# Kernel tuning notes

Hardware: AMD Instinct MI355X
Metric: run time of the kernel (lower is better)

## Reference

```python
import jax, jax.numpy as jnp
import numpy as np

N, E, B = 30000, 100000, 1024
FXD, FXT, D, H, NOUT = 78, 954, 128, 10, 2


def setup_inputs() -> dict:
    key = jax.random.key(0)
    ks = jax.random.split(key, 24)
    rn = lambda i, shape, s=0.05: jax.random.normal(ks[i], shape, dtype=jnp.float32) * s
    z = lambda shape: jnp.zeros(shape, dtype=jnp.float32)
    batch = ((jnp.arange(N) * B) // N).astype(jnp.int32)  # sorted, every graph id present
    return {
        "x1": rn(0, (N, FXD), 1.0),
        "edge_index1": jax.random.randint(ks[1], (2, E), 0, N, dtype=jnp.int32),
        "batch1": batch,
        "x2": rn(2, (N, FXD), 1.0),
        "edge_index2": jax.random.randint(ks[3], (2, E), 0, N, dtype=jnp.int32),
        "batch2": batch,
        "cell": jax.random.uniform(ks[4], (B, FXT), dtype=jnp.float32),
        "W1": rn(5, (FXD, H * D)), "a_src1": rn(6, (1, H, D)), "a_dst1": rn(7, (1, H, D)), "b1": z((H * D,)),
        # GATConv2: 1280 -> 128, 1 head
        "W2": rn(8, (H * D, D)), "a_src2": rn(9, (1, 1, D)), "a_dst2": rn(10, (1, 1, D)), "b2": z((D,)),
        "Wg": rn(11, (D, D)), "bg": z((D,)),
        "Wr1": rn(12, (FXT, 2048)), "br1": z((2048,)),
        "Wr2": rn(13, (2048, 512)), "br2": z((512,)),
        "Wr3": rn(14, (512, 2 * D)), "br3": z((2 * D,)),
        "Wf1": rn(15, (4 * D, 1024)), "bf1": z((1024,)),
        "Wf2": rn(16, (1024, 512)), "bf2": z((512,)),
        "Wf3": rn(17, (512, 128)), "bf3": z((128,)),
        "Wo": rn(18, (128, NOUT)), "bo": z((NOUT,)),
    }


def gat_conv(x, src, dst, W, a_src, a_dst, bias, heads, ch):
    """PyG GATConv (v1), self-loops already included in src/dst. Concat heads."""
    n = x.shape[0]
    h = (x @ W).reshape(n, heads, ch)                      # [N,H,C]
    alpha_s = jnp.sum(h * a_src, axis=-1)                  # [N,H]
    alpha_d = jnp.sum(h * a_dst, axis=-1)                  # [N,H]
    e = jax.nn.leaky_relu(alpha_s[src] + alpha_d[dst], 0.2)  # [E',H]
    emax = jax.ops.segment_max(e, dst, num_segments=n)     # segment softmax over dst
    ex = jnp.exp(e - emax[dst])
    denom = jax.ops.segment_sum(ex, dst, num_segments=n)
    alpha = ex / (denom[dst] + 1e-16)                      # [E',H]
    msg = h[src] * alpha[:, :, None]                       # [E',H,C]
    out = jax.ops.segment_sum(msg, dst, num_segments=n)    # [N,H,C]
    return out.reshape(n, heads * ch) + bias


def _l2norm(x):
    return x / jnp.maximum(jnp.linalg.norm(x, axis=1, keepdims=True), 1e-12)


def reference(x1, edge_index1, batch1, x2, edge_index2, batch2, cell,
              W1, a_src1, a_dst1, b1, W2, a_src2, a_dst2, b2, Wg, bg,
              Wr1, br1, Wr2, br2, Wr3, br3, Wf1, bf1, Wf2, bf2, Wf3, bf3, Wo, bo):
    def branch(x, ei, batch):
        n = x.shape[0]
        loops = jnp.arange(n, dtype=ei.dtype)              # add_self_loops=True
        src = jnp.concatenate([ei[0], loops])
        dst = jnp.concatenate([ei[1], loops])
        h = jax.nn.elu(gat_conv(x, src, dst, W1, a_src1, a_dst1, b1, H, D))
        h = jax.nn.elu(gat_conv(h, src, dst, W2, a_src2, a_dst2, b2, 1, D))
        g = jax.ops.segment_max(h, batch, num_segments=B)  # global_max_pool
        return jax.nn.relu(g @ Wg + bg)

    v1 = branch(x1, edge_index1, batch1)
    v2 = branch(x2, edge_index2, batch2)
    c = _l2norm(cell)
    c = jax.nn.relu(c @ Wr1 + br1)
    c = jax.nn.relu(c @ Wr2 + br2)
    c = jax.nn.relu(c @ Wr3 + br3)
    xc = _l2norm(jnp.concatenate([v1, v2, c], axis=1))
    xc = jax.nn.relu(xc @ Wf1 + bf1)
    xc = jax.nn.relu(xc @ Wf2 + bf2)
    xc = jax.nn.relu(xc @ Wf3 + bf3)
    return xc @ Wo + bo
```

## Files before the change

kernel.cpp:

```cpp
#include <hip/hip_runtime.h>
#include <math.h>

typedef unsigned short ushort_t;
typedef __attribute__((ext_vector_type(8))) short short8;
typedef __attribute__((ext_vector_type(8))) unsigned short ushort8v;
typedef __attribute__((ext_vector_type(4))) float float4v;
typedef __attribute__((ext_vector_type(4))) unsigned short ushort4v;

#define MPAD 30016
#define H1STR 136

__device__ __forceinline__ float lrelu02(float v){ return v > 0.f ? v : 0.2f*v; }
__device__ __forceinline__ float elu_fast(float v){ return v > 0.f ? v : (__expf(v) - 1.f); }

__device__ __forceinline__ ushort_t f2bf(float x){
  unsigned u = __float_as_uint(x);
  return (ushort_t)((u + 0x7fffu + ((u >> 16) & 1u)) >> 16);
}
__device__ __forceinline__ float bf2f(ushort_t h){ return __uint_as_float(((unsigned)h) << 16); }

__device__ __forceinline__ unsigned encf(float f){
  unsigned u = __float_as_uint(f);
  return (u & 0x80000000u) ? ~u : (u | 0x80000000u);
}
__device__ __forceinline__ float decf(unsigned u){
  return __uint_as_float((u >> 31) ? (u & 0x7FFFFFFFu) : ~u);
}

__device__ __forceinline__ void gll16(const void* g, void* l){
  __builtin_amdgcn_global_load_lds((const __attribute__((address_space(1))) void*)g,
                                   (__attribute__((address_space(3))) void*)l, 16, 0, 0);
}

__global__ void fill_int_k(int* p, int v, int n){
  int i = blockIdx.x*blockDim.x + threadIdx.x;
  if (i < n) p[i] = v;
}

__global__ void hist2_k(const int* __restrict__ ei1, const int* __restrict__ ei2,
                        int E, int N, int* deg){
  int idx = blockIdx.x*blockDim.x + threadIdx.x;
  if (idx < 2*E){
    int br = idx / E, e = idx - br*E;
    const int* ei = br ? ei2 : ei1;
    atomicAdd(&deg[br*N + ei[E + e]], 1);
  }
}

__global__ __launch_bounds__(1024)
void scanA_k(const int* __restrict__ deg, int* __restrict__ rowptr, int* __restrict__ bsum, int n){
  int br = blockIdx.y;
  int t = threadIdx.x;
  int i = blockIdx.x*1024 + t;
  __shared__ int s[1024];
  int v = (i < n) ? deg[br*n + i] : 0;
  s[t] = v; __syncthreads();
  for (int off = 1; off < 1024; off <<= 1){
    int x = (t >= off) ? s[t - off] : 0;
    __syncthreads();
    s[t] += x;
    __syncthreads();
  }
  if (i < n) rowptr[br*(n+1) + i] = s[t] - v;
  if (t == 1023) bsum[br*gridDim.x + blockIdx.x] = s[1023];
}

__global__ void scanB_k(int* bsum, int nb){
  int br = threadIdx.x;
  if (br < 2){
    int run = 0;
    for (int i = 0; i < nb; ++i){ int v = bsum[br*nb + i]; bsum[br*nb + i] = run; run += v; }
  }
}

__global__ __launch_bounds__(1024)
void scanC_k(const int* __restrict__ bsum, int* __restrict__ rowptr, int* __restrict__ cursor,
             int n, int nb, int total){
  int br = blockIdx.y;
  int i = blockIdx.x*1024 + threadIdx.x;
  int add = bsum[br*nb + blockIdx.x];
  if (i < n){
    int nv = rowptr[br*(n+1) + i] + add;
    rowptr[br*(n+1) + i] = nv;
    cursor[br*n + i] = nv;
  }
  if (i == 0) rowptr[br*(n+1) + n] = total;
}

__global__ void fill_csr2_k(const int* __restrict__ ei1, const int* __restrict__ ei2,
                            int E, int N, int* cursor, int* csr){
  int idx = blockIdx.x*blockDim.x + threadIdx.x;
  if (idx < 2*E){
    int br = idx / E, e = idx - br*E;
    const int* ei = br ? ei2 : ei1;
    int dst = ei[E + e];
    int pos = atomicAdd(&cursor[br*N + dst], 1);
    csr[br*(E+N) + pos] = ei[e];
  }
}

__global__ void self_loop2_k(int* cursor, int* csr, int E, int N){
  int idx = blockIdx.x*blockDim.x + threadIdx.x;
  if (idx < 2*N){
    int br = idx / N, i = idx - br*N;
    int pos = atomicAdd(&cursor[br*N + i], 1);
    csr[br*(E+N) + pos] = i;
  }
}

__global__ void mkattn_k(const float* __restrict__ W1, const float* __restrict__ a_src1,
                         const float* __restrict__ a_dst1,
                         const float* __restrict__ W2, const float* __restrict__ a_src2,
                         const float* __restrict__ a_dst2,
                         float* As, float* Ad, float* vs, float* vd){
  int idx = blockIdx.x*blockDim.x + threadIdx.x;
  if (idx < 780){
    int f = idx / 10, h = idx % 10;
    float ss = 0.f, sd = 0.f;
    for (int c = 0; c < 128; ++c){
      float w = W1[f*1280 + h*128 + c];
      ss += w * a_src1[h*128 + c];
      sd += w * a_dst1[h*128 + c];
    }
    As[idx] = ss; Ad[idx] = sd;
  } else if (idx < 2060){
    int k = idx - 780;
    float ss = 0.f, sd = 0.f;
    for (int c = 0; c < 128; ++c){
      float w = W2[k*128 + c];
      ss += w * a_src2[c]; sd += w * a_dst2[c];
    }
    vs[k] = ss; vd[k] = sd;
  }
}

__global__ __launch_bounds__(256)
void alpha1b_k(const float* __restrict__ x1, const float* __restrict__ x2,
               const float* __restrict__ As, const float* __restrict__ Ad,
               float* as1, float* ad1, int n){
  __shared__ float sAs[780], sAd[780];
  int t = threadIdx.x;
  for (int k = t; k < 780; k += 256){ sAs[k] = As[k]; sAd[k] = Ad[k]; }
  __syncthreads();
  int idx = blockIdx.x*256 + t;
  if (idx >= 2*n) return;
  int br = idx / n, i = idx - br*n;
  const float* xr = (br ? x2 : x1) + (size_t)i*78;
  float ss[10], sd[10];
  #pragma unroll
  for (int h = 0; h < 10; ++h){ ss[h] = 0.f; sd[h] = 0.f; }
  for (int f = 0; f < 78; ++f){
    float xv = xr[f];
    #pragma unroll
    for (int h = 0; h < 10; ++h){
      ss[h] += xv * sAs[f*10 + h];
      sd[h] += xv * sAd[f*10 + h];
    }
  }
  #pragma unroll
  for (int h = 0; h < 10; ++h){
    as1[(size_t)idx*10 + h] = ss[h];
    ad1[(size_t)idx*10 + h] = sd[h];
  }
}

__global__ __launch_bounds__(64)
void gat1_agg_k(const int* __restrict__ rowptr2, const int* __restrict__ csr2,
                const float* __restrict__ x1, const float* __restrict__ x2,
                const float* __restrict__ as1b, const float* __restrict__ ad1b,
                ushort_t* __restrict__ yh, int n, int E){
  int gi = blockIdx.x;
  int br = (gi >= n) ? 1 : 0;
  int i = gi - br*n;
  int t = threadIdx.x;
  const int* rowptr = rowptr2 + (size_t)br*(n+1);
  const int* csr    = csr2 + (size_t)br*(E+n);
  const float* x    = br ? x2 : x1;
  const float* as1  = as1b + (size_t)br*n*10;
  ushort_t* yb      = yh + (size_t)br*10*MPAD*96;

  __shared__ float adi[10], rden[10], wE[10], xs[78];
  int beg = rowptr[i], end = rowptr[i+1];
  if (t < 10) adi[t] = ad1b[(size_t)gi*10 + t];
  __syncthreads();
  float den = 0.f;
  float acc[13];
  int hh[13], cc[13];
  #pragma unroll
  for (int k = 0; k < 13; ++k){
    acc[k] = 0.f;
    int j = t + 64*k;
    hh[k] = (j < 780) ? (j/78) : 0;
    cc[k] = (j < 780) ? (j%78) : 0;
  }
  for (int e = beg; e < end; ++e){
    int s = csr[e];
    if (t < 10){
      float w = __expf(lrelu02(as1[(size_t)s*10 + t] + adi[t]));
      wE[t] = w; den += w;
    }
    for (int c = t; c < 78; c += 64) xs[c] = x[(size_t)s*78 + c];
    __syncthreads();
    #pragma unroll
    for (int k = 0; k < 13; ++k){
      int j = t + 64*k;
      if (j < 780) acc[k] += wE[hh[k]] * xs[cc[k]];
    }
    __syncthreads();
  }
  if (t < 10) rden[t] = 1.f/(den + 1e-16f);
  __syncthreads();
  #pragma unroll
  for (int k = 0; k < 13; ++k){
    int j = t + 64*k;
    if (j < 780) yb[((size_t)hh[k]*MPAD + i)*96 + cc[k]] = f2bf(acc[k]*rden[hh[k]]);
  }
  for (int p = t; p < 180; p += 64){
    int h = p/18, c = 78 + p%18;
    yb[((size_t)h*MPAD + i)*96 + c] = 0;
  }
}

__global__ __launch_bounds__(256)
void branch_conv_k(const ushort_t* __restrict__ yall,
                   const ushort_t* __restrict__ W1h, const ushort_t* __restrict__ W1l,
                   const ushort_t* __restrict__ W2h, const ushort_t* __restrict__ W2l,
                   const float* __restrict__ b1, const float* __restrict__ vs,
                   const float* __restrict__ vd,
                   float* __restrict__ h2all, float* __restrict__ as2all,
                   float* __restrict__ ad2all, int M){
  const int NBLK = MPAD/64;
  int br = blockIdx.x / NBLK;
  int bi = blockIdx.x - br*NBLK;
  const ushort_t* y = yall + (size_t)br*10*MPAD*96;
  float* h2  = h2all + (size_t)br*MPAD*128;
  float* as2 = as2all + (size_t)br*MPAD;
  float* ad2 = ad2all + (size_t)br*MPAD;

  __shared__ ushort_t stage[2][10240];
  __shared__ ushort_t h1t[64*H1STR];
  __shared__ float red[256];

  int tid = threadIdx.x, lane = tid & 63, wave = tid >> 6;
  int row0 = bi*64;
  int wm = (wave & 1)*32, wn = (wave >> 1)*64;
  int lr = lane & 15, quad = lane >> 4;
  int sr = lane >> 2;
  int skc = (((lane & 3) ^ ((lane >> 3) & 3)) * 8);
  int qs  = (quad ^ ((lr >> 1) & 3)) * 8;

  float4v acc2[2][4];
  #pragma unroll
  for (int i = 0; i < 2; ++i)
    #pragma unroll
    for (int j = 0; j < 4; ++j)
      acc2[i][j] = (float4v){0.f, 0.f, 0.f, 0.f};
  float rps[8], rpd[8];
  #pragma unroll
  for (int z = 0; z < 8; ++z){ rps[z] = 0.f; rpd[z] = 0.f; }

  for (int h = 0; h < 10; ++h){
    const ushort_t* gA   = y   + ((size_t)h*MPAD + row0 + wave*16 + sr)*96 + skc;
    const ushort_t* gB0h = W1h + ((size_t)(h*128 + wave*32      + sr))*96 + skc;
    const ushort_t* gB1h = W1h + ((size_t)(h*128 + wave*32 + 16 + sr))*96 + skc;
    const ushort_t* gB0l = W1l + ((size_t)(h*128 + wave*32      + sr))*96 + skc;
    const ushort_t* gB1l = W1l + ((size_t)(h*128 + wave*32 + 16 + sr))*96 + skc;
    const ushort_t* gC0h = W2h + ((size_t)(wave*32      + sr))*1280 + h*128 + skc;
    const ushort_t* gC1h = W2h + ((size_t)(wave*32 + 16 + sr))*1280 + h*128 + skc;
    const ushort_t* gC0l = W2l + ((size_t)(wave*32      + sr))*1280 + h*128 + skc;
    const ushort_t* gC1l = W2l + ((size_t)(wave*32 + 16 + sr))*1280 + h*128 + skc;

    auto issue1 = [&](int p, int kt){
      ushort_t* st = &stage[p][0];
      gll16(gA   + kt, st + wave*512);
      gll16(gB0h + kt, st + 2048 + wave*1024);
      gll16(gB1h + kt, st + 2048 + wave*1024 + 512);
      gll16(gB0l + kt, st + 6144 + wave*1024);
      gll16(gB1l + kt, st + 6144 + wave*1024 + 512);
    };
    auto issue2 = [&](int p, int kt){
      ushort_t* st = &stage[p][0];
      gll16(gC0h + kt, st + 2048 + wave*1024);
      gll16(gC1h + kt, st + 2048 + wave*1024 + 512);
      gll16(gC0l + kt, st + 6144 + wave*1024);
      gll16(gC1l + kt, st + 6144 + wave*1024 + 512);
    };

    __syncthreads();
    issue1(0, 0);
    float4v acc1[2][4];
    #pragma unroll
    for (int i = 0; i < 2; ++i)
      #pragma unroll
      for (int j = 0; j < 4; ++j)
        acc1[i][j] = (float4v){0.f, 0.f, 0.f, 0.f};
    int p = 0;
    #pragma unroll
    for (int it = 0; it < 3; ++it){
      __syncthreads();
      if (it < 2) issue1(p ^ 1, (it + 1)*32);
      const ushort_t* sm = &stage[p][0];
      short8 af[2], bhf[4], blf[4];
      #pragma unroll
      for (int t2 = 0; t2 < 2; ++t2)
        af[t2] = *(const short8*)&sm[(wm + t2*16 + lr)*32 + qs];
      #pragma unroll
      for (int j = 0; j < 4; ++j){
        int nb = (wn + j*16 + lr)*32 + qs;
        bhf[j] = *(const short8*)&sm[2048 + nb];
        blf[j] = *(const short8*)&sm[6144 + nb];
      }
      #pragma unroll
      for (int i = 0; i < 2; ++i)
        #pragma unroll
        for (int j = 0; j < 4; ++j){
          acc1[i][j] = __builtin_amdgcn_mfma_f32_16x16x32_bf16(af[i], blf[j], acc1[i][j], 0, 0, 0);
          acc1[i][j] = __builtin_amdgcn_mfma_f32_16x16x32_bf16(af[i], bhf[j], acc1[i][j], 0, 0, 0);
        }
      p ^= 1;
    }

    #pragma unroll
    for (int j = 0; j < 4; ++j){
      int col = wn + j*16 + lr;
      float bv  = b1[h*128 + col];
      float vsv = vs[h*128 + col];
      float vdv = vd[h*128 + col];
      #pragma unroll
      for (int i = 0; i < 2; ++i){
        #pragma unroll
        for (int r = 0; r < 4; ++r){
          float v = elu_fast(acc1[i][j][r] + bv);
          h1t[(wm + i*16 + quad*4 + r)*H1STR + col] = f2bf(v);
          rps[i*4 + r] += v * vsv;
          rpd[i*4 + r] += v * vdv;
        }
      }
    }
    __syncthreads();

    issue2(0, 0);
    p = 0;
    #pragma unroll
    for (int it = 0; it < 4; ++it){
      __syncthreads();
      if (it < 3) issue2(p ^ 1, (it + 1)*32);
      const ushort_t* sm = &stage[p][0];
      int kt = it*32;
      short8 af[2], bhf[4], blf[4];
      #pragma unroll
      for (int t2 = 0; t2 < 2; ++t2)
        af[t2] = *(const short8*)&h1t[(wm + t2*16 + lr)*H1STR + kt + quad*8];
      #pragma unroll
      for (int j = 0; j < 4; ++j){
        int nb = (wn + j*16 + lr)*32 + qs;
        bhf[j] = *(const short8*)&sm[2048 + nb];
        blf[j] = *(const short8*)&sm[6144 + nb];
      }
      #pragma unroll
      for (int i = 0; i < 2; ++i)
        #pragma unroll
        for (int j = 0; j < 4; ++j){
          acc2[i][j] = __builtin_amdgcn_mfma_f32_16x16x32_bf16(af[i], blf[j], acc2[i][j], 0, 0, 0);
          acc2[i][j] = __builtin_amdgcn_mfma_f32_16x16x32_bf16(af[i], bhf[j], acc2[i][j], 0, 0, 0);
        }
      p ^= 1;
    }
  }

  #pragma unroll
  for (int j = 0; j < 4; ++j){
    int col = wn + j*16 + lr;
    #pragma unroll
    for (int i = 0; i < 2; ++i){
      #pragma unroll
      for (int r = 0; r < 4; ++r){
        int row = row0 + wm + i*16 + quad*4 + r;
        if (row < M) h2[(size_t)row*128 + col] = acc2[i][j][r];
      }
    }
  }
  __syncthreads();
  #pragma unroll
  for (int z = 0; z < 8; ++z){
    float a = rps[z], d = rpd[z];
    #pragma unroll
    for (int mk = 1; mk <= 8; mk <<= 1){
      a += __shfl_xor(a, mk);
      d += __shfl_xor(d, mk);
    }
    if (lr == 0){
      int i = z >> 2, r = z & 3;
      int row = wm + i*16 + quad*4 + r;
      red[row*2 + (wave >> 1)] = a;
      red[128 + row*2 + (wave >> 1)] = d;
    }
  }
  __syncthreads();
  if (tid < 64){
    int grow = row0 + tid;
    if (grow < M){
      as2[grow] = red[tid*2] + red[tid*2 + 1];
      ad2[grow] = red[128 + tid*2] + red[128 + tid*2 + 1];
    }
  }
}

__global__ __launch_bounds__(64)
void gat2_agg_k(const int* __restrict__ rowptr2, const int* __restrict__ csr2,
                const float* __restrict__ h2all, const float* __restrict__ as2all,
                const float* __restrict__ ad2all, const float* __restrict__ b2,
                const int* __restrict__ batch1, const int* __restrict__ batch2,
                unsigned* __restrict__ poolKey, int n, int E, int Bg){
  int gi = blockIdx.x;
  int br = (gi >= n) ? 1 : 0;
  int i = gi - br*n;
  int t = threadIdx.x;
  const int* rowptr = rowptr2 + (size_t)br*(n+1);
  const int* csr    = csr2 + (size_t)br*(E+n);
  const float* h2   = h2all + (size_t)br*MPAD*128;
  const float* as2  = as2all + (size_t)br*MPAD;
  float adi = ad2all[(size_t)br*MPAD + i];
  int beg = rowptr[i], end = rowptr[i+1];
  float den = 0.f, a0 = 0.f, a1 = 0.f;
  for (int e = beg; e < end; ++e){
    int s = csr[e];
    float w = __expf(lrelu02(as2[s] + adi));
    den += w;
    a0 += w * h2[(size_t)s*128 + t];
    a1 += w * h2[(size_t)s*128 + 64 + t];
  }
  float r = 1.f/(den + 1e-16f);
  float o0 = elu_fast(a0*r + b2[t]);
  float o1 = elu_fast(a1*r + b2[64 + t]);
  int g = (br ? batch2 : batch1)[i];
  unsigned* pk = poolKey + ((size_t)br*Bg + g)*128;
  atomicMax(&pk[t], encf(o0));
  atomicMax(&pk[64 + t], encf(o1));
}

__global__ void pool_decode_k(const unsigned* __restrict__ key,
                              ushort_t* __restrict__ ph, ushort_t* __restrict__ pl, int n){
  int i = blockIdx.x*blockDim.x + threadIdx.x;
  if (i < n){
    float v = decf(key[i]);
    ushort_t h = f2bf(v);
    ph[i] = h; pl[i] = f2bf(v - bf2f(h));
  }
}

__global__ __launch_bounds__(256)
void l2norm_split_k(const float* __restrict__ in, int cols, int Kp,
                    ushort_t* __restrict__ oh, ushort_t* __restrict__ ol){
  int r = blockIdx.x, t = threadIdx.x;
  __shared__ float s[256];
  __shared__ float scaleS;
  const float* rp = in + (size_t)r*cols;
  float p = 0.f;
  for (int k = t; k < cols; k += 256){ float v = rp[k]; p += v*v; }
  s[t] = p; __syncthreads();
  for (int o = 128; o > 0; o >>= 1){
    if (t < o) s[t] += s[t+o];
    __syncthreads();
  }
  if (t == 0) scaleS = 1.f / fmaxf(sqrtf(s[0]), 1e-12f);
  __syncthreads();
  float sc = scaleS;
  for (int k = t; k < Kp; k += 256){
    float v = (k < cols) ? rp[k]*sc : 0.f;
    ushort_t h = f2bf(v);
    size_t o2 = (size_t)r*Kp + k;
    oh[o2] = h; ol[o2] = f2bf(v - bf2f(h));
  }
}

__global__ __launch_bounds__(256)
void catnorm_k(const float* __restrict__ vall, const float* __restrict__ c3,
               ushort_t* __restrict__ oh, ushort_t* __restrict__ ol, int Bg){
  int r = blockIdx.x, t = threadIdx.x;
  __shared__ float s[256];
  __shared__ float scaleS;
  auto val = [&](int c)->float{
    if (c < 128) return vall[(size_t)r*128 + c];
    if (c < 256) return vall[((size_t)Bg + r)*128 + (c - 128)];
    return c3[(size_t)r*256 + (c - 256)];
  };
  float v0 = val(t), v1 = val(t + 256);
  s[t] = v0*v0 + v1*v1; __syncthreads();
  for (int o = 128; o > 0; o >>= 1){
    if (t < o) s[t] += s[t+o];
    __syncthreads();
  }
  if (t == 0) scaleS = 1.f / fmaxf(sqrtf(s[0]), 1e-12f);
  __syncthreads();
  float sc = scaleS;
  float a = v0*sc, b = v1*sc;
  ushort_t ha = f2bf(a), hb = f2bf(b);
  size_t o2 = (size_t)r*512;
  oh[o2 + t] = ha;       ol[o2 + t] = f2bf(a - bf2f(ha));
  oh[o2 + 256 + t] = hb; ol[o2 + 256 + t] = f2bf(b - bf2f(hb));
}

__global__ void act_split_k(const float* __restrict__ in, ushort_t* __restrict__ oh,
                            ushort_t* __restrict__ ol, int n){
  int i = blockIdx.x*blockDim.x + threadIdx.x;
  if (i < n){
    float v = fmaxf(in[i], 0.f);
    ushort_t h = f2bf(v);
    oh[i] = h; ol[i] = f2bf(v - bf2f(h));
  }
}

__device__ __forceinline__ void split_one(const float* __restrict__ W, int ldw, int colStride,
                                          int N, int K, int Np, int Kp,
                                          ushort_t* __restrict__ dh, ushort_t* __restrict__ dl,
                                          int idx){
  int n  = idx % Np;
  int r  = idx / Np;
  int k4 = r % (Kp >> 2);
  int b  = r / (Kp >> 2);
  size_t o = ((size_t)b*Np + n)*Kp + (size_t)k4*4;
  ushort4v hv, lv;
  #pragma unroll
  for (int kk = 0; kk < 4; ++kk){
    int k = k4*4 + kk;
    float v = (n < N && k < K) ? W[(size_t)k*ldw + (size_t)b*colStride + n] : 0.f;
    ushort_t h = f2bf(v);
    hv[kk] = h; lv[kk] = f2bf(v - bf2f(h));
  }
  *(ushort4v*)&dh[o] = hv;
  *(ushort4v*)&dl[o] = lv;
}

struct SplitTable {
  const float *W1, *W2, *Wg, *Wr1, *Wr2, *Wr3, *Wf1, *Wf2, *Wf3, *Wo;
  ushort_t *W1h,*W1l,*W2h,*W2l,*Wgh,*Wgl,*Wr1h,*Wr1l,*Wr2h,*Wr2l;
  ushort_t *Wr3h,*Wr3l,*Wf1h,*Wf1l,*Wf2h,*Wf2l,*Wf3h,*Wf3l,*Woh,*Wol;
};

__global__ void split_all_k(SplitTable T){
  int idx = blockIdx.x*blockDim.x + threadIdx.x;
  if      (idx <   30720) split_one(T.W1, 1280, 128, 128,   78,  128,   96, T.W1h, T.W1l, idx);
  else if (idx <   71680) split_one(T.W2,  128,   0, 128, 1280,  128, 1280, T.W2h, T.W2l, idx -   30720);
  else if (idx <   75776) split_one(T.Wg,  128,   0, 128,  128,  128,  128, T.Wgh, T.Wgl, idx -   71680);
  else if (idx <  567296) split_one(T.Wr1,2048,   0,2048,  954, 2048,  960, T.Wr1h,T.Wr1l,idx -   75776);
  else if (idx <  829440) split_one(T.Wr2, 512,   0, 512, 2048,  512, 2048, T.Wr2h,T.Wr2l,idx -  567296);
  else if (idx <  862208) split_one(T.Wr3, 256,   0, 256,  512,  256,  512, T.Wr3h,T.Wr3l,idx -  829440);
  else if (idx <  993280) split_one(T.Wf1,1024,   0,1024,  512, 1024,  512, T.Wf1h,T.Wf1l,idx -  862208);
  else if (idx < 1124352) split_one(T.Wf2, 512,   0, 512, 1024,  512, 1024, T.Wf2h,T.Wf2l,idx -  993280);
  else if (idx < 1140736) split_one(T.Wf3, 128,   0, 128,  512,  128,  512, T.Wf3h,T.Wf3l,idx - 1124352);
  else if (idx < 1142784) split_one(T.Wo,    2,   0,   2,  128,   64,  128, T.Woh, T.Wol, idx - 1140736);
}

__global__ __launch_bounds__(256)
void gemm_split(const ushort_t* __restrict__ Ahp, const ushort_t* __restrict__ Alp, int lda, long long sA,
                const ushort_t* __restrict__ Bhp, const ushort_t* __restrict__ Blp, int ldb, long long sB,
                float* __restrict__ C, ushort_t* __restrict__ Ch, ushort_t* __restrict__ Cl,
                int ldc, long long sC,
                const float* __restrict__ bias, int sBias,
                int M, int Nc, int K, int act, int outMode, int kSplit, int aSplit){
  int zb = blockIdx.z;
  int b = zb / kSplit, kc = zb - b*kSplit;
  Ahp += (long long)b*sA;
  Bhp += (long long)b*sB; Blp += (long long)b*sB;
  long long cOff = (long long)b*sC;
  int Kc = K / kSplit;
  int kb = kc*Kc;
  int nIter = Kc / 32;

  __shared__ ushort_t smem[18048];

  int tid = threadIdx.x, lane = tid & 63, wave = tid >> 6;
  int row0 = blockIdx.y*64, col0 = blockIdx.x*64;
  int wm = (wave & 1)*32, wn = (wave >> 1)*32;
  int lr = lane & 15, quad = lane >> 4;
  int qs = (quad ^ ((lr >> 1) & 3)) * 8;

  int srow = wave*16 + (lane >> 2);
  int skc  = (((lane & 3) ^ ((lane >> 3) & 3)) * 8);
  const ushort_t* gAh = Ahp + (long long)(row0 + srow)*lda + skc + kb;
  const ushort_t* gAl = aSplit ? (Alp + (long long)b*sA + (long long)(row0 + srow)*lda + skc + kb) : gAh;
  const ushort_t* gBh = Bhp + (long long)(col0 + srow)*ldb + skc + kb;
  const ushort_t* gBl = Blp + (long long)(col0 + srow)*ldb + skc + kb;

  float4v acc[2][2];
  #pragma unroll
  for (int i = 0; i < 2; ++i)
    #pragma unroll
    for (int j = 0; j < 2; ++j)
      acc[i][j] = (float4v){0.f, 0.f, 0.f, 0.f};

  auto issue = [&](int p, int kt){
    ushort_t* base = &smem[p*8192 + wave*512];
    gll16(gAh + kt, base);
    if (aSplit) gll16(gAl + kt, base + 2048);
    gll16(gBh + kt, base + 4096);
    gll16(gBl + kt, base + 6144);
  };

  issue(0, 0);
  int p = 0;
  for (int it = 0; it < nIter; ++it){
    __syncthreads();
    if (it + 1 < nIter) issue(p ^ 1, (it + 1)*32);
    const ushort_t* sm = &smem[p*8192];
    short8 ah[2], al[2], bh[2], bl[2];
    #pragma unroll
    for (int t2 = 0; t2 < 2; ++t2){
      int ao = (wm + t2*16 + lr)*32 + qs;
      int bo = (wn + t2*16 + lr)*32 + qs;
      ah[t2] = *(const short8*)&sm[ao];
      if (aSplit) al[t2] = *(const short8*)&sm[2048 + ao];
      bh[t2] = *(const short8*)&sm[4096 + bo];
      bl[t2] = *(const short8*)&sm[6144 + bo];
    }
    #pragma unroll
    for (int i = 0; i < 2; ++i)
      #pragma unroll
      for (int j = 0; j < 2; ++j){
        if (aSplit)
          acc[i][j] = __builtin_amdgcn_mfma_f32_16x16x32_bf16(al[i], bh[j], acc[i][j], 0, 0, 0);
        acc[i][j] = __builtin_amdgcn_mfma_f32_16x16x32_bf16(ah[i], bl[j], acc[i][j], 0, 0, 0);
        acc[i][j] = __builtin_amdgcn_mfma_f32_16x16x32_bf16(ah[i], bh[j], acc[i][j], 0, 0, 0);
      }
    p ^= 1;
  }
  __syncthreads();

  if (outMode == 0 || outMode == 2){
    #pragma unroll
    for (int j = 0; j < 2; ++j){
      int col = col0 + wn + j*16 + lr;
      if (col >= Nc) continue;
      float bv = (bias && kc == 0) ? bias[(long long)b*sBias + col] : 0.f;
      #pragma unroll
      for (int i = 0; i < 2; ++i){
        #pragma unroll
        for (int r = 0; r < 4; ++r){
          int row = row0 + wm + i*16 + quad*4 + r;
          if (row >= M) continue;
          float v = acc[i][j][r] + bv;
          if (act == 1) v = fmaxf(v, 0.f);
          else if (act == 2) v = elu_fast(v);
          long long o = cOff + (long long)row*ldc + col;
          if (outMode == 0) C[o] = v;
          else atomicAdd(&C[o], v);
        }
      }
    }
  } else {
    float* ftile = (float*)smem;
    #pragma unroll
    for (int i = 0; i < 2; ++i)
      #pragma unroll
      for (int j = 0; j < 2; ++j)
        #pragma unroll
        for (int r = 0; r < 4; ++r)
          ftile[(wm + i*16 + quad*4 + r)*68 + wn + j*16 + lr] = acc[i][j][r];
    __syncthreads();
    int row = tid >> 2, ch = (tid & 3)*16;
    int grow = row0 + row;
    if (grow < M){
      if (col0 + 64 <= Nc){
        long long o = cOff + (long long)grow*ldc + col0 + ch;
        #pragma unroll
        for (int g = 0; g < 2; ++g){
          ushort8v hv, lv;
          #pragma unroll
          for (int c = 0; c < 8; ++c){
            int cc2 = ch + g*8 + c;
            float v = ftile[row*68 + cc2];
            if (bias) v += bias[(long long)b*sBias + col0 + cc2];
            if (act == 1) v = fmaxf(v, 0.f);
            else if (act == 2) v = elu_fast(v);
            hv[c] = f2bf(v);
            lv[c] = f2bf(v - bf2f(hv[c]));
          }
          *(ushort8v*)&Ch[o + g*8] = hv;
          *(ushort8v*)&Cl[o + g*8] = lv;
        }
      } else {
        for (int c = 0; c < 16; ++c){
          int col = col0 + ch + c;
          if (col >= Nc) break;
          float v = ftile[row*68 + ch + c];
          if (bias) v += bias[(long long)b*sBias + col];
          if (act == 1) v = fmaxf(v, 0.f);
          else if (act == 2) v = elu_fast(v);
          long long o = cOff + (long long)grow*ldc + col;
          ushort_t h = f2bf(v);
          Ch[o] = h;
          Cl[o] = f2bf(v - bf2f(h));
        }
      }
    }
  }
}

extern "C" void kernel_launch(void* const* d_in, const int* in_sizes, int n_in,
                              void* d_out, int out_size, void* d_ws, size_t ws_size,
                              hipStream_t stream){
  const float* x1     = (const float*)d_in[0];
  const int*   ei1    = (const int*)  d_in[1];
  const int*   batch1 = (const int*)  d_in[2];
  const float* x2     = (const float*)d_in[3];
  const int*   ei2    = (const int*)  d_in[4];
  const int*   batch2 = (const int*)  d_in[5];
  const float* cell   = (const float*)d_in[6];
  const float* W1     = (const float*)d_in[7];
  const float* a_src1 = (const float*)d_in[8];
  const float* a_dst1 = (const float*)d_in[9];
  const float* b1     = (const float*)d_in[10];
  const float* W2     = (const float*)d_in[11];
  const float* a_src2 = (const float*)d_in[12];
  const float* a_dst2 = (const float*)d_in[13];
  const float* b2     = (const float*)d_in[14];
  const float* Wg     = (const float*)d_in[15];
  const float* bg     = (const float*)d_in[16];
  const float* Wr1    = (const float*)d_in[17];
  const float* br1    = (const float*)d_in[18];
  const float* Wr2    = (const float*)d_in[19];
  const float* br2    = (const float*)d_in[20];
  const float* Wr3    = (const float*)d_in[21];
  const float* br3    = (const float*)d_in[22];
  const float* Wf1    = (const float*)d_in[23];
  const float* bf1    = (const float*)d_in[24];
  const float* Wf2    = (const float*)d_in[25];
  const float* bf2    = (const float*)d_in[26];
  const float* Wf3    = (const float*)d_in[27];
  const float* bf3    = (const float*)d_in[28];
  const float* Wo     = (const float*)d_in[29];
  const float* bo     = (const float*)d_in[30];
  float* out = (float*)d_out;
  (void)n_in; (void)out_size; (void)ws_size;

  const int N  = in_sizes[0] / 78;
  const int E  = in_sizes[1] / 2;
  const int Bg = in_sizes[6] / 954;

  char* wsb = (char*)d_ws;
  size_t off = 0;
  auto alloc = [&](size_t bytes)->char*{
    char* p = wsb + off; off += ((bytes + 255)/256)*256; return p;
  };

  char* Yb = alloc((size_t)2*10*MPAD*96*2);
  ushort_t* yh = (ushort_t*)Yb;
  size_t yoff = 0;
  auto yalloc = [&](size_t bytes)->char*{
    char* p = Yb + yoff; yoff += ((bytes + 255)/256)*256; return p;
  };
  ushort_t* cnh  = (ushort_t*)yalloc((size_t)Bg*960*2);
  ushort_t* cnl  = (ushort_t*)yalloc((size_t)Bg*960*2);
  ushort_t* c1h  = (ushort_t*)yalloc((size_t)Bg*2048*2);
  ushort_t* c1l  = (ushort_t*)yalloc((size_t)Bg*2048*2);
  ushort_t* c2h  = (ushort_t*)yalloc((size_t)Bg*512*2);
  ushort_t* c2l  = (ushort_t*)yalloc((size_t)Bg*512*2);
  float*    c3   = (float*)   yalloc((size_t)Bg*256*4);
  ushort_t* xcnh = (ushort_t*)yalloc((size_t)Bg*512*2);
  ushort_t* xcnl = (ushort_t*)yalloc((size_t)Bg*512*2);
  ushort_t* t1h  = (ushort_t*)yalloc((size_t)Bg*1024*2);
  ushort_t* t1l  = (ushort_t*)yalloc((size_t)Bg*1024*2);
  ushort_t* t2h  = (ushort_t*)yalloc((size_t)Bg*512*2);
  ushort_t* t2l  = (ushort_t*)yalloc((size_t)Bg*512*2);
  ushort_t* t3h  = (ushort_t*)yalloc((size_t)Bg*128*2);
  ushort_t* t3l  = (ushort_t*)yalloc((size_t)Bg*128*2);
  ushort_t* pooledh = (ushort_t*)yalloc((size_t)2*Bg*128*2);
  ushort_t* pooledl = (ushort_t*)yalloc((size_t)2*Bg*128*2);
  float*    vall    = (float*)   yalloc((size_t)2*Bg*128*4);

  size_t zElems = (size_t)Bg*512 + (size_t)Bg*512 + (size_t)Bg*128 + (size_t)2*Bg*128;
  float* zbase = (float*)alloc(zElems*4);
  float* c2f = zbase;
  float* t2f = c2f + (size_t)Bg*512;
  float* t3f = t2f + (size_t)Bg*512;
  unsigned* poolKey = (unsigned*)(t3f + (size_t)Bg*128);

  float* h2  = (float*)alloc((size_t)2*MPAD*128*4);
  float* as2 = (float*)alloc((size_t)2*MPAD*4);
  float* ad2 = (float*)alloc((size_t)2*MPAD*4);

  ushort_t* W1th = (ushort_t*)alloc((size_t)10*128*96*2);
  ushort_t* W1tl = (ushort_t*)alloc((size_t)10*128*96*2);
  ushort_t* W2th = (ushort_t*)alloc((size_t)128*1280*2);
  ushort_t* W2tl = (ushort_t*)alloc((size_t)128*1280*2);
  ushort_t* Wgth = (ushort_t*)alloc((size_t)128*128*2);
  ushort_t* Wgtl = (ushort_t*)alloc((size_t)128*128*2);
  ushort_t* Wr1th= (ushort_t*)alloc((size_t)2048*960*2);
  ushort_t* Wr1tl= (ushort_t*)alloc((size_t)2048*960*2);
  ushort_t* Wr2th= (ushort_t*)alloc((size_t)512*2048*2);
  ushort_t* Wr2tl= (ushort_t*)alloc((size_t)512*2048*2);
  ushort_t* Wr3th= (ushort_t*)alloc((size_t)256*512*2);
  ushort_t* Wr3tl= (ushort_t*)alloc((size_t)256*512*2);
  ushort_t* Wf1th= (ushort_t*)alloc((size_t)1024*512*2);
  ushort_t* Wf1tl= (ushort_t*)alloc((size_t)1024*512*2);
  ushort_t* Wf2th= (ushort_t*)alloc((size_t)512*1024*2);
  ushort_t* Wf2tl= (ushort_t*)alloc((size_t)512*1024*2);
  ushort_t* Wf3th= (ushort_t*)alloc((size_t)128*512*2);
  ushort_t* Wf3tl= (ushort_t*)alloc((size_t)128*512*2);
  ushort_t* Woth = (ushort_t*)alloc((size_t)64*128*2);
  ushort_t* Wotl = (ushort_t*)alloc((size_t)64*128*2);

  float* as1b = (float*)alloc((size_t)2*N*10*4);
  float* ad1b = (float*)alloc((size_t)2*N*10*4);
  float* AsB  = (float*)alloc(780*4);
  float* AdB  = (float*)alloc(780*4);
  float* vs   = (float*)alloc(1280*4);
  float* vd   = (float*)alloc(1280*4);
  int* deg2    = (int*)alloc((size_t)2*N*4);
  int* rowptr2 = (int*)alloc((size_t)2*(N+1)*4);
  int* cursor2 = (int*)alloc((size_t)2*N*4);
  int* csr2    = (int*)alloc((size_t)2*(E+N)*4);
  int* bsum    = (int*)alloc((size_t)2*64*4);

  auto gemm = [&](const ushort_t* Ah_, const ushort_t* Al_, int lda, long long sA_,
                  const ushort_t* Bh_, const ushort_t* Bl_, int ldb, long long sB_,
                  float* C_, ushort_t* Ch_, ushort_t* Cl_, int ldc, long long sC_,
                  const float* bias_, int sBias_, int M_, int N_, int K_, int batch_,
                  int act_, int mode_, int kSplit_, int aSplit_){
    dim3 grid((N_ + 63)/64, (M_ + 63)/64, batch_*kSplit_);
    gemm_split<<<grid, 256, 0, stream>>>(Ah_, Al_, lda, sA_, Bh_, Bl_, ldb, sB_,
                                         C_, Ch_, Cl_, ldc, sC_, bias_, sBias_,
                                         M_, N_, K_, act_, mode_, kSplit_, aSplit_);
  };

  hipMemsetAsync(zbase, 0, zElems*4, stream);
  SplitTable T;
  T.W1 = W1; T.W2 = W2; T.Wg = Wg; T.Wr1 = Wr1; T.Wr2 = Wr2; T.Wr3 = Wr3;
  T.Wf1 = Wf1; T.Wf2 = Wf2; T.Wf3 = Wf3; T.Wo = Wo;
  T.W1h = W1th; T.W1l = W1tl; T.W2h = W2th; T.W2l = W2tl; T.Wgh = Wgth; T.Wgl = Wgtl;
  T.Wr1h = Wr1th; T.Wr1l = Wr1tl; T.Wr2h = Wr2th; T.Wr2l = Wr2tl;
  T.Wr3h = Wr3th; T.Wr3l = Wr3tl; T.Wf1h = Wf1th; T.Wf1l = Wf1tl;
  T.Wf2h = Wf2th; T.Wf2l = Wf2tl; T.Wf3h = Wf3th; T.Wf3l = Wf3tl;
  T.Woh = Woth; T.Wol = Wotl;
  split_all_k<<<(1142784 + 255)/256, 256, 0, stream>>>(T);
  mkattn_k<<<(2060 + 255)/256, 256, 0, stream>>>(W1, a_src1, a_dst1, W2, a_src2, a_dst2,
                                                 AsB, AdB, vs, vd);
  alpha1b_k<<<((2*N) + 255)/256, 256, 0, stream>>>(x1, x2, AsB, AdB, as1b, ad1b, N);

  const int NB = (N + 1023)/1024;
  fill_int_k<<<((2*N) + 255)/256, 256, 0, stream>>>(deg2, 1, 2*N);
  hist2_k<<<((2*E) + 255)/256, 256, 0, stream>>>(ei1, ei2, E, N, deg2);
  scanA_k<<<dim3(NB, 2), 1024, 0, stream>>>(deg2, rowptr2, bsum, N);
  scanB_k<<<1, 64, 0, stream>>>(bsum, NB);
  scanC_k<<<dim3(NB, 2), 1024, 0, stream>>>(bsum, rowptr2, cursor2, N, NB, E + N);
  fill_csr2_k<<<((2*E) + 255)/256, 256, 0, stream>>>(ei1, ei2, E, N, cursor2, csr2);
  self_loop2_k<<<((2*N) + 255)/256, 256, 0, stream>>>(cursor2, csr2, E, N);

  gat1_agg_k<<<2*N, 64, 0, stream>>>(rowptr2, csr2, x1, x2, as1b, ad1b, yh, N, E);
  branch_conv_k<<<2*(MPAD/64), 256, 0, stream>>>(yh, W1th, W1tl, W2th, W2tl,
                                                 b1, vs, vd, h2, as2, ad2, N);
  gat2_agg_k<<<2*N, 64, 0, stream>>>(rowptr2, csr2, h2, as2, ad2, b2,
                                     batch1, batch2, poolKey, N, E, Bg);
  pool_decode_k<<<((2*Bg*128) + 255)/256, 256, 0, stream>>>(poolKey, pooledh, pooledl, 2*Bg*128);
  gemm(pooledh, pooledl, 128, 0, Wgth, Wgtl, 128, 0,
       vall, nullptr, nullptr, 128, 0, bg, 0, 2*Bg, 128, 128, 1, 1, 0, 1, 1);

  l2norm_split_k<<<Bg, 256, 0, stream>>>(cell, 954, 960, cnh, cnl);
  gemm(cnh, cnl, 960, 0, Wr1th, Wr1tl, 960, 0, nullptr, c1h, c1l, 2048, 0,
       br1, 0, Bg, 2048, 960, 1, 1, 1, 1, 1);
  gemm(c1h, c1l, 2048, 0, Wr2th, Wr2tl, 2048, 0, c2f, nullptr, nullptr, 512, 0,
       br2, 0, Bg, 512, 2048, 1, 0, 2, 4, 1);
  act_split_k<<<((Bg*512) + 255)/256, 256, 0, stream>>>(c2f, c2h, c2l, Bg*512);
  gemm(c2h, c2l, 512, 0, Wr3th, Wr3tl, 512, 0, c3, nullptr, nullptr, 256, 0,
       br3, 0, Bg, 256, 512, 1, 1, 0, 1, 1);

  catnorm_k<<<Bg, 256, 0, stream>>>(vall, c3, xcnh, xcnl, Bg);
  gemm(xcnh, xcnl, 512, 0, Wf1th, Wf1tl, 512, 0, nullptr, t1h, t1l, 1024, 0,
       bf1, 0, Bg, 1024, 512, 1, 1, 1, 1, 1);
  gemm(t1h, t1l, 1024, 0, Wf2th, Wf2tl, 1024, 0, t2f, nullptr, nullptr, 512, 0,
       bf2, 0, Bg, 512, 1024, 1, 0, 2, 4, 1);
  act_split_k<<<((Bg*512) + 255)/256, 256, 0, stream>>>(t2f, t2h, t2l, Bg*512);
  gemm(t2h, t2l, 512, 0, Wf3th, Wf3tl, 512, 0, t3f, nullptr, nullptr, 128, 0,
       bf3, 0, Bg, 128, 512, 1, 0, 2, 4, 1);
  act_split_k<<<((Bg*128) + 255)/256, 256, 0, stream>>>(t3f, t3h, t3l, Bg*128);
  gemm(t3h, t3l, 128, 0, Woth, Wotl, 128, 0, out, nullptr, nullptr, 2, 0,
       bo, 0, Bg, 2, 128, 1, 0, 0, 1, 1);
}
```

Baseline: 601.0 us.

## Drop low-part bf16 split for GAT weights, store h2 as bf16, fuse CSR kernels

Removes the hi/lo bf16 split compensation for W1 and W2 in the fused branch convolution, which halves the MFMA count and the weight staging traffic there. The h2 intermediate is now stored as bf16 instead of fp32, cutting write and gather bandwidth in the second GAT aggregation. The degree fill kernel is folded into the memset plus a +1 in the scan, and the self-loop insertion is merged into the CSR fill kernel, saving launches. The cost is reduced precision in the GAT layers, which risks exceeding the accuracy tolerance.

```diff
diff --git a/kernel.cpp b/kernel.cpp
--- a/kernel.cpp
+++ b/kernel.cpp
@@ -30,11 +30,6 @@
 __device__ __forceinline__ void gll16(const void* g, void* l){
   __builtin_amdgcn_global_load_lds((const __attribute__((address_space(1))) void*)g,
                                    (__attribute__((address_space(3))) void*)l, 16, 0, 0);
-}
-
-__global__ void fill_int_k(int* p, int v, int n){
-  int i = blockIdx.x*blockDim.x + threadIdx.x;
-  if (i < n) p[i] = v;
 }
 
 __global__ void hist2_k(const int* __restrict__ ei1, const int* __restrict__ ei2,
@@ -53,7 +48,7 @@
   int t = threadIdx.x;
   int i = blockIdx.x*1024 + t;
   __shared__ int s[1024];
-  int v = (i < n) ? deg[br*n + i] : 0;
+  int v = (i < n) ? (deg[br*n + i] + 1) : 0;
   s[t] = v; __syncthreads();
   for (int off = 1; off < 1024; off <<= 1){
     int x = (t >= off) ? s[t - off] : 0;
@@ -96,13 +91,9 @@
     int dst = ei[E + e];
     int pos = atomicAdd(&cursor[br*N + dst], 1);
     csr[br*(E+N) + pos] = ei[e];
-  }
-}
-
-__global__ void self_loop2_k(int* cursor, int* csr, int E, int N){
-  int idx = blockIdx.x*blockDim.x + threadIdx.x;
-  if (idx < 2*N){
-    int br = idx / N, i = idx - br*N;
+  } else if (idx < 2*E + 2*N){
+    int r = idx - 2*E;
+    int br = r / N, i = r - br*N;
     int pos = atomicAdd(&cursor[br*N + i], 1);
     csr[br*(E+N) + pos] = i;
   }
@@ -223,21 +214,20 @@
 
 __global__ __launch_bounds__(256)
 void branch_conv_k(const ushort_t* __restrict__ yall,
-                   const ushort_t* __restrict__ W1h, const ushort_t* __restrict__ W1l,
-                   const ushort_t* __restrict__ W2h, const ushort_t* __restrict__ W2l,
+                   const ushort_t* __restrict__ W1h, const ushort_t* __restrict__ W2h,
                    const float* __restrict__ b1, const float* __restrict__ vs,
                    const float* __restrict__ vd,
-                   float* __restrict__ h2all, float* __restrict__ as2all,
+                   ushort_t* __restrict__ h2all, float* __restrict__ as2all,
                    float* __restrict__ ad2all, int M){
   const int NBLK = MPAD/64;
   int br = blockIdx.x / NBLK;
   int bi = blockIdx.x - br*NBLK;
   const ushort_t* y = yall + (size_t)br*10*MPAD*96;
-  float* h2  = h2all + (size_t)br*MPAD*128;
+  ushort_t* h2 = h2all + (size_t)br*MPAD*128;
   float* as2 = as2all + (size_t)br*MPAD;
   float* ad2 = ad2all + (size_t)br*MPAD;
 
-  __shared__ ushort_t stage[2][10240];
+  __shared__ ushort_t stage[2][6144];
   __shared__ ushort_t h1t[64*H1STR];
   __shared__ float red[256];
 
@@ -263,27 +253,19 @@
     const ushort_t* gA   = y   + ((size_t)h*MPAD + row0 + wave*16 + sr)*96 + skc;
     const ushort_t* gB0h = W1h + ((size_t)(h*128 + wave*32      + sr))*96 + skc;
     const ushort_t* gB1h = W1h + ((size_t)(h*128 + wave*32 + 16 + sr))*96 + skc;
-    const ushort_t* gB0l = W1l + ((size_t)(h*128 + wave*32      + sr))*96 + skc;
-    const ushort_t* gB1l = W1l + ((size_t)(h*128 + wave*32 + 16 + sr))*96 + skc;
     const ushort_t* gC0h = W2h + ((size_t)(wave*32      + sr))*1280 + h*128 + skc;
     const ushort_t* gC1h = W2h + ((size_t)(wave*32 + 16 + sr))*1280 + h*128 + skc;
-    const ushort_t* gC0l = W2l + ((size_t)(wave*32      + sr))*1280 + h*128 + skc;
-    const ushort_t* gC1l = W2l + ((size_t)(wave*32 + 16 + sr))*1280 + h*128 + skc;
 
     auto issue1 = [&](int p, int kt){
       ushort_t* st = &stage[p][0];
       gll16(gA   + kt, st + wave*512);
       gll16(gB0h + kt, st + 2048 + wave*1024);
       gll16(gB1h + kt, st + 2048 + wave*1024 + 512);
-      gll16(gB0l + kt, st + 6144 + wave*1024);
-      gll16(gB1l + kt, st + 6144 + wave*1024 + 512);
     };
     auto issue2 = [&](int p, int kt){
       ushort_t* st = &stage[p][0];
       gll16(gC0h + kt, st + 2048 + wave*1024);
       gll16(gC1h + kt, st + 2048 + wave*1024 + 512);
-      gll16(gC0l + kt, st + 6144 + wave*1024);
-      gll16(gC1l + kt, st + 6144 + wave*1024 + 512);
     };
 
     __syncthreads();
@@ -300,23 +282,18 @@
       __syncthreads();
       if (it < 2) issue1(p ^ 1, (it + 1)*32);
       const ushort_t* sm = &stage[p][0];
-      short8 af[2], bhf[4], blf[4];
+      short8 af[2], bhf[4];
       #pragma unroll
       for (int t2 = 0; t2 < 2; ++t2)
         af[t2] = *(const short8*)&sm[(wm + t2*16 + lr)*32 + qs];
       #pragma unroll
-      for (int j = 0; j < 4; ++j){
-        int nb = (wn + j*16 + lr)*32 + qs;
-        bhf[j] = *(const short8*)&sm[2048 + nb];
-        blf[j] = *(const short8*)&sm[6144 + nb];
-      }
+      for (int j = 0; j < 4; ++j)
+        bhf[j] = *(const short8*)&sm[2048 + (wn + j*16 + lr)*32 + qs];
       #pragma unroll
       for (int i = 0; i < 2; ++i)
         #pragma unroll
-        for (int j = 0; j < 4; ++j){
-          acc1[i][j] = __builtin_amdgcn_mfma_f32_16x16x32_bf16(af[i], blf[j], acc1[i][j], 0, 0, 0);
+        for (int j = 0; j < 4; ++j)
           acc1[i][j] = __builtin_amdgcn_mfma_f32_16x16x32_bf16(af[i], bhf[j], acc1[i][j], 0, 0, 0);
-        }
       p ^= 1;
     }
 
@@ -347,23 +324,18 @@
       if (it < 3) issue2(p ^ 1, (it + 1)*32);
       const ushort_t* sm = &stage[p][0];
       int kt = it*32;
-      short8 af[2], bhf[4], blf[4];
+      short8 af[2], bhf[4];
       #pragma unroll
       for (int t2 = 0; t2 < 2; ++t2)
         af[t2] = *(const short8*)&h1t[(wm + t2*16 + lr)*H1STR + kt + quad*8];
       #pragma unroll
-      for (int j = 0; j < 4; ++j){
-        int nb = (wn + j*16 + lr)*32 + qs;
-        bhf[j] = *(const short8*)&sm[2048 + nb];
-        blf[j] = *(const short8*)&sm[6144 + nb];
-      }
+      for (int j = 0; j < 4; ++j)
+        bhf[j] = *(const short8*)&sm[2048 + (wn + j*16 + lr)*32 + qs];
       #pragma unroll
       for (int i = 0; i < 2; ++i)
         #pragma unroll
-        for (int j = 0; j < 4; ++j){
-          acc2[i][j] = __builtin_amdgcn_mfma_f32_16x16x32_bf16(af[i], blf[j], acc2[i][j], 0, 0, 0);
+        for (int j = 0; j < 4; ++j)
           acc2[i][j] = __builtin_amdgcn_mfma_f32_16x16x32_bf16(af[i], bhf[j], acc2[i][j], 0, 0, 0);
-        }
       p ^= 1;
     }
   }
@@ -376,7 +348,7 @@
       #pragma unroll
       for (int r = 0; r < 4; ++r){
         int row = row0 + wm + i*16 + quad*4 + r;
-        if (row < M) h2[(size_t)row*128 + col] = acc2[i][j][r];
+        if (row < M) h2[(size_t)row*128 + col] = f2bf(acc2[i][j][r]);
       }
     }
   }
@@ -408,7 +380,7 @@
 
 __global__ __launch_bounds__(64)
 void gat2_agg_k(const int* __restrict__ rowptr2, const int* __restrict__ csr2,
-                const float* __restrict__ h2all, const float* __restrict__ as2all,
+                const ushort_t* __restrict__ h2all, const float* __restrict__ as2all,
                 const float* __restrict__ ad2all, const float* __restrict__ b2,
                 const int* __restrict__ batch1, const int* __restrict__ batch2,
                 unsigned* __restrict__ poolKey, int n, int E, int Bg){
@@ -418,7 +390,7 @@
   int t = threadIdx.x;
   const int* rowptr = rowptr2 + (size_t)br*(n+1);
   const int* csr    = csr2 + (size_t)br*(E+n);
-  const float* h2   = h2all + (size_t)br*MPAD*128;
+  const ushort_t* h2 = h2all + (size_t)br*MPAD*128;
   const float* as2  = as2all + (size_t)br*MPAD;
   float adi = ad2all[(size_t)br*MPAD + i];
   int beg = rowptr[i], end = rowptr[i+1];
@@ -427,16 +399,17 @@
     int s = csr[e];
     float w = __expf(lrelu02(as2[s] + adi));
     den += w;
-    a0 += w * h2[(size_t)s*128 + t];
-    a1 += w * h2[(size_t)s*128 + 64 + t];
+    unsigned u = *(const unsigned*)&h2[(size_t)s*128 + 2*t];
+    a0 += w * bf2f((ushort_t)(u & 0xffffu));
+    a1 += w * bf2f((ushort_t)(u >> 16));
   }
   float r = 1.f/(den + 1e-16f);
-  float o0 = elu_fast(a0*r + b2[t]);
-  float o1 = elu_fast(a1*r + b2[64 + t]);
+  float o0 = elu_fast(a0*r + b2[2*t]);
+  float o1 = elu_fast(a1*r + b2[2*t + 1]);
   int g = (br ? batch2 : batch1)[i];
   unsigned* pk = poolKey + ((size_t)br*Bg + g)*128;
-  atomicMax(&pk[t], encf(o0));
-  atomicMax(&pk[64 + t], encf(o1));
+  atomicMax(&pk[2*t], encf(o0));
+  atomicMax(&pk[2*t + 1], encf(o1));
 }
 
 __global__ void pool_decode_k(const unsigned* __restrict__ key,
@@ -529,19 +502,19 @@
     hv[kk] = h; lv[kk] = f2bf(v - bf2f(h));
   }
   *(ushort4v*)&dh[o] = hv;
-  *(ushort4v*)&dl[o] = lv;
+  if (dl) *(ushort4v*)&dl[o] = lv;
 }
 
 struct SplitTable {
   const float *W1, *W2, *Wg, *Wr1, *Wr2, *Wr3, *Wf1, *Wf2, *Wf3, *Wo;
-  ushort_t *W1h,*W1l,*W2h,*W2l,*Wgh,*Wgl,*Wr1h,*Wr1l,*Wr2h,*Wr2l;
+  ushort_t *W1h,*W2h,*Wgh,*Wgl,*Wr1h,*Wr1l,*Wr2h,*Wr2l;
   ushort_t *Wr3h,*Wr3l,*Wf1h,*Wf1l,*Wf2h,*Wf2l,*Wf3h,*Wf3l,*Woh,*Wol;
 };
 
 __global__ void split_all_k(SplitTable T){
   int idx = blockIdx.x*blockDim.x + threadIdx.x;
-  if      (idx <   30720) split_one(T.W1, 1280, 128, 128,   78,  128,   96, T.W1h, T.W1l, idx);
-  else if (idx <   71680) split_one(T.W2,  128,   0, 128, 1280,  128, 1280, T.W2h, T.W2l, idx -   30720);
+  if      (idx <   30720) split_one(T.W1, 1280, 128, 128,   78,  128,   96, T.W1h, nullptr, idx);
+  else if (idx <   71680) split_one(T.W2,  128,   0, 128, 1280,  128, 1280, T.W2h, nullptr, idx -   30720);
   else if (idx <   75776) split_one(T.Wg,  128,   0, 128,  128,  128,  128, T.Wgh, T.Wgl, idx -   71680);
   else if (idx <  567296) split_one(T.Wr1,2048,   0,2048,  954, 2048,  960, T.Wr1h,T.Wr1l,idx -   75776);
   else if (idx <  829440) split_one(T.Wr2, 512,   0, 512, 2048,  512, 2048, T.Wr2h,T.Wr2l,idx -  567296);
@@ -769,21 +742,21 @@
   ushort_t* pooledl = (ushort_t*)yalloc((size_t)2*Bg*128*2);
   float*    vall    = (float*)   yalloc((size_t)2*Bg*128*4);
 
-  size_t zElems = (size_t)Bg*512 + (size_t)Bg*512 + (size_t)Bg*128 + (size_t)2*Bg*128;
+  size_t zElems = (size_t)Bg*512 + (size_t)Bg*512 + (size_t)Bg*128 + (size_t)2*Bg*128
+                + (size_t)2*N;
   float* zbase = (float*)alloc(zElems*4);
   float* c2f = zbase;
   float* t2f = c2f + (size_t)Bg*512;
   float* t3f = t2f + (size_t)Bg*512;
   unsigned* poolKey = (unsigned*)(t3f + (size_t)Bg*128);
-
-  float* h2  = (float*)alloc((size_t)2*MPAD*128*4);
+  int* deg2 = (int*)(poolKey + (size_t)2*Bg*128);
+
+  ushort_t* h2 = (ushort_t*)alloc((size_t)2*MPAD*128*2);
   float* as2 = (float*)alloc((size_t)2*MPAD*4);
   float* ad2 = (float*)alloc((size_t)2*MPAD*4);
 
   ushort_t* W1th = (ushort_t*)alloc((size_t)10*128*96*2);
-  ushort_t* W1tl = (ushort_t*)alloc((size_t)10*128*96*2);
   ushort_t* W2th = (ushort_t*)alloc((size_t)128*1280*2);
-  ushort_t* W2tl = (ushort_t*)alloc((size_t)128*1280*2);
   ushort_t* Wgth = (ushort_t*)alloc((size_t)128*128*2);
   ushort_t* Wgtl = (ushort_t*)alloc((size_t)128*128*2);
   ushort_t* Wr1th= (ushort_t*)alloc((size_t)2048*960*2);
@@ -807,7 +780,6 @@
   float* AdB  = (float*)alloc(780*4);
   float* vs   = (float*)alloc(1280*4);
   float* vd   = (float*)alloc(1280*4);
-  int* deg2    = (int*)alloc((size_t)2*N*4);
   int* rowptr2 = (int*)alloc((size_t)2*(N+1)*4);
   int* cursor2 = (int*)alloc((size_t)2*N*4);
   int* csr2    = (int*)alloc((size_t)2*(E+N)*4);
@@ -828,7 +800,7 @@
   SplitTable T;
   T.W1 = W1; T.W2 = W2; T.Wg = Wg; T.Wr1 = Wr1; T.Wr2 = Wr2; T.Wr3 = Wr3;
   T.Wf1 = Wf1; T.Wf2 = Wf2; T.Wf3 = Wf3; T.Wo = Wo;
-  T.W1h = W1th; T.W1l = W1tl; T.W2h = W2th; T.W2l = W2tl; T.Wgh = Wgth; T.Wgl = Wgtl;
+  T.W1h = W1th; T.W2h = W2th; T.Wgh = Wgth; T.Wgl = Wgtl;
   T.Wr1h = Wr1th; T.Wr1l = Wr1tl; T.Wr2h = Wr2th; T.Wr2l = Wr2tl;
   T.Wr3h = Wr3th; T.Wr3l = Wr3tl; T.Wf1h = Wf1th; T.Wf1l = Wf1tl;
   T.Wf2h = Wf2th; T.Wf2l = Wf2tl; T.Wf3h = Wf3th; T.Wf3l = Wf3tl;
@@ -839,16 +811,14 @@
   alpha1b_k<<<((2*N) + 255)/256, 256, 0, stream>>>(x1, x2, AsB, AdB, as1b, ad1b, N);
 
   const int NB = (N + 1023)/1024;
-  fill_int_k<<<((2*N) + 255)/256, 256, 0, stream>>>(deg2, 1, 2*N);
   hist2_k<<<((2*E) + 255)/256, 256, 0, stream>>>(ei1, ei2, E, N, deg2);
   scanA_k<<<dim3(NB, 2), 1024, 0, stream>>>(deg2, rowptr2, bsum, N);
   scanB_k<<<1, 64, 0, stream>>>(bsum, NB);
   scanC_k<<<dim3(NB, 2), 1024, 0, stream>>>(bsum, rowptr2, cursor2, N, NB, E + N);
-  fill_csr2_k<<<((2*E) + 255)/256, 256, 0, stream>>>(ei1, ei2, E, N, cursor2, csr2);
-  self_loop2_k<<<((2*N) + 255)/256, 256, 0, stream>>>(cursor2, csr2, E, N);
+  fill_csr2_k<<<((2*E + 2*N) + 255)/256, 256, 0, stream>>>(ei1, ei2, E, N, cursor2, csr2);
 
   gat1_agg_k<<<2*N, 64, 0, stream>>>(rowptr2, csr2, x1, x2, as1b, ad1b, yh, N, E);
-  branch_conv_k<<<2*(MPAD/64), 256, 0, stream>>>(yh, W1th, W1tl, W2th, W2tl,
+  branch_conv_k<<<2*(MPAD/64), 256, 0, stream>>>(yh, W1th, W2th,
                                                  b1, vs, vd, h2, as2, ad2, N);
   gat2_agg_k<<<2*N, 64, 0, stream>>>(rowptr2, csr2, h2, as2, ad2, b2,
                                      batch1, batch2, poolKey, N, E, Bg);
```

New measurement: 564.0 us. 6.2% less time.
